# Kernel optimization log

Measured on AMD Instinct MI355X. Metric: run time of the kernel, lower is better.

The kernel has to match this reference:

```python
import jax, jax.numpy as jnp
import numpy as np

# Model constants (match init_kwargs)
H = 16       # num query heads
HKV = 8      # num kv heads
G = H // HKV # group size for GQA
D = 128      # head_dim
EPS = 1e-06
THETA = 10000.0
SCALE = D ** -0.5


def setup_inputs() -> dict:
    key = jax.random.key(0)
    k1, k2, k3 = jax.random.split(key, 3)
    T, HID = 2048, 2048
    qkv_out = H * D + 2 * HKV * D  # 4096
    return {
        "x": jax.random.normal(k1, (T, HID), jnp.float32),
        "pos": jnp.arange(T, dtype=jnp.int64 if jax.config.jax_enable_x64 else jnp.int32),
        "w_qkv": jax.random.normal(k2, (HID, qkv_out), jnp.float32) * 0.02,
        "q_norm_w": jnp.ones((D,), jnp.float32),
        "k_norm_w": jnp.ones((D,), jnp.float32),
        "w_o": jax.random.normal(k3, (H * D, HID), jnp.float32) * 0.02,
    }


def _rmsnorm(x, w):
    # per-head RMSNorm over last dim (head_dim)
    var = jnp.mean(jnp.square(x), axis=-1, keepdims=True)
    return x * jax.lax.rsqrt(var + EPS) * w


def _rope(x, pos):
    # neox-style rotary: rotate_half over full head_dim
    inv_freq = 1.0 / (THETA ** (jnp.arange(0, D, 2, dtype=jnp.float32) / D))  # [D/2]
    ang = pos.astype(jnp.float32)[:, None] * inv_freq                          # [T, D/2]
    cos = jnp.concatenate([jnp.cos(ang), jnp.cos(ang)], -1)[:, None, :]        # [T,1,D]
    sin = jnp.concatenate([jnp.sin(ang), jnp.sin(ang)], -1)[:, None, :]
    x1, x2 = x[..., : D // 2], x[..., D // 2 :]
    rot = jnp.concatenate([-x2, x1], -1)
    return x * cos + rot * sin


def reference(x, pos, w_qkv, q_norm_w, k_norm_w, w_o):
    T = x.shape[0]
    qkv = x @ w_qkv                                   # [T, (H+2*HKV)*D]
    q = qkv[:, : H * D].reshape(T, H, D)
    k = qkv[:, H * D : (H + HKV) * D].reshape(T, HKV, D)
    v = qkv[:, (H + HKV) * D :].reshape(T, HKV, D)
    q = _rmsnorm(q, q_norm_w)
    k = _rmsnorm(k, k_norm_w)
    q = _rope(q, pos)
    k = _rope(k, pos)
    # GQA causal attention over a single flattened sequence
    qg = q.reshape(T, HKV, G, D)
    scores = jnp.einsum("qhgd,khd->hgqk", qg, k) * SCALE   # [HKV,G,T,T]
    causal = pos[:, None] >= pos[None, :]                   # [T,T]
    scores = jnp.where(causal, scores, jnp.finfo(scores.dtype).min)
    probs = jax.nn.softmax(scores, axis=-1)
    o = jnp.einsum("hgqk,khd->qhgd", probs, v).reshape(T, H * D)
    return o @ w_o
```

## Files before the change

kernel.cpp:

```cpp
#include <hip/hip_runtime.h>
#include <hip/hip_bf16.h>
#include <math.h>

#define T_SEQ 2048
#define HID   2048
#define NH    16
#define NKV   8
#define DH    128
#define QKV_N 4096
#define KOFF  2048
#define VOFF  3072
#define EPS_RMS 1e-6f
#define ATT_SCALE 0.08838834764831845f

typedef __attribute__((ext_vector_type(8))) short bf16x8;
typedef __attribute__((ext_vector_type(4))) float f32x4;
typedef unsigned short u16;

__device__ __forceinline__ u16 f2b(float f) {
  union { float f; unsigned u; } v; v.f = f;
  unsigned r = v.u + 0x7fff + ((v.u >> 16) & 1);
  return (u16)(r >> 16);
}
__device__ __forceinline__ float b2f(u16 x) {
  union { unsigned u; float f; } v; v.u = ((unsigned)x) << 16;
  return v.f;
}

__device__ __forceinline__ void g2l16(u16* l, const u16* g) {
#if __has_builtin(__builtin_amdgcn_global_load_lds)
  __builtin_amdgcn_global_load_lds(
      (const __attribute__((address_space(1))) unsigned int*)g,
      (__attribute__((address_space(3))) unsigned int*)l, 16, 0, 0);
#else
  *(float4*)l = *(const float4*)g;
#endif
}

__global__ __launch_bounds__(256)
void cast_bf16(const float* __restrict__ src, u16* __restrict__ dst) {
  const int i = blockIdx.x * 256 + threadIdx.x;
  const float4 v = ((const float4*)src)[i];
  ushort4 o; o.x = f2b(v.x); o.y = f2b(v.y); o.z = f2b(v.z); o.w = f2b(v.w);
  ((ushort4*)dst)[i] = o;
}

__global__ __launch_bounds__(256)
void tcast(const float* __restrict__ src, u16* __restrict__ dst, int R, int C) {
  __shared__ u16 tile[32][36];
  const int br = blockIdx.y * 32, bc = blockIdx.x * 32;
  const int t = threadIdx.x;
  {
    const int r = t >> 3, c4 = (t & 7) * 4;
    const float4 v = *(const float4*)(src + (size_t)(br + r) * C + bc + c4);
    tile[c4 + 0][r] = f2b(v.x);
    tile[c4 + 1][r] = f2b(v.y);
    tile[c4 + 2][r] = f2b(v.z);
    tile[c4 + 3][r] = f2b(v.w);
  }
  __syncthreads();
  {
    const int c = t >> 3, r4 = (t & 7) * 4;
    ushort4 o = { tile[c][r4], tile[c][r4 + 1], tile[c][r4 + 2], tile[c][r4 + 3] };
    *(ushort4*)(dst + (size_t)(bc + c) * R + br + r4) = o;
  }
}

template<int BOUT>
__global__ __launch_bounds__(256)
void gemm_bt(const u16* __restrict__ A, const u16* __restrict__ BT,
             void* __restrict__ Cout, int M, int N, int K) {
  __shared__ u16 sA[128 * 32];
  __shared__ u16 sB[128 * 32];

  const int t = threadIdx.x;
  const int lane = t & 63, wv = t >> 6;
  const int lo = lane & 15, hi = lane >> 4;
  const int bm = blockIdx.y * 128, bn = blockIdx.x * 128;
  const int wr = (wv >> 1) * 64, wc = (wv & 1) * 64;

  f32x4 acc[4][4];
#pragma unroll
  for (int m = 0; m < 4; ++m)
#pragma unroll
    for (int n = 0; n < 4; ++n) acc[m][n] = (f32x4){0.f, 0.f, 0.f, 0.f};

  const int arow = wv * 32 + (lane >> 2);
  const int koff = (lane & 3) * 8;
  const u16* gA = A + (size_t)(bm + arow) * K + koff;
  const u16* gB = BT + (size_t)(bn + arow) * K + koff;
  u16* lA = sA + wv * 1024 + lane * 8;
  u16* lB = sB + wv * 1024 + lane * 8;

  for (int k0 = 0; k0 < K; k0 += 32) {
    g2l16(lA,       gA + k0);
    g2l16(lA + 512, gA + (size_t)16 * K + k0);
    g2l16(lB,       gB + k0);
    g2l16(lB + 512, gB + (size_t)16 * K + k0);
    __syncthreads();

    bf16x8 af[4], bfr[4];
#pragma unroll
    for (int m = 0; m < 4; ++m)
      af[m] = *(const bf16x8*)(sA + (wr + m * 16 + lo) * 32 + hi * 8);
#pragma unroll
    for (int n = 0; n < 4; ++n)
      bfr[n] = *(const bf16x8*)(sB + (wc + n * 16 + lo) * 32 + hi * 8);
#pragma unroll
    for (int m = 0; m < 4; ++m)
#pragma unroll
      for (int n = 0; n < 4; ++n)
        acc[m][n] = __builtin_amdgcn_mfma_f32_16x16x32_bf16(af[m], bfr[n], acc[m][n], 0, 0, 0);
    __syncthreads();
  }

#pragma unroll
  for (int m = 0; m < 4; ++m)
#pragma unroll
    for (int n = 0; n < 4; ++n)
#pragma unroll
      for (int r = 0; r < 4; ++r) {
        const int row = bm + wr + m * 16 + hi * 4 + r;
        const int col = bn + wc + n * 16 + lo;
        if constexpr (BOUT)
          ((u16*)Cout)[(size_t)row * N + col] = f2b(acc[m][n][r]);
        else
          ((float*)Cout)[(size_t)row * N + col] = acc[m][n][r];
      }
}

__global__ __launch_bounds__(256)
void normrope(const u16* __restrict__ qkvb, const int* __restrict__ pos,
              const float* __restrict__ qw, const float* __restrict__ kw,
              u16* __restrict__ qbf, u16* __restrict__ kbf) {
  const int wv = threadIdx.x >> 6, lane = threadIdx.x & 63;
  const int idx = blockIdx.x * 4 + wv;
  const int tt = idx / 24, hh = idx % 24;

  const int off = (hh < NH) ? hh * DH : KOFF + (hh - NH) * DH;
  const u16* base = qkvb + (size_t)tt * QKV_N + off;
  const float x1 = b2f(base[lane]);
  const float x2 = b2f(base[lane + 64]);

  float ss = x1 * x1 + x2 * x2;
#pragma unroll
  for (int o = 32; o > 0; o >>= 1) ss += __shfl_xor(ss, o);

  const float inv = rsqrtf(ss * (1.0f / DH) + EPS_RMS);
  const float* w = (hh < NH) ? qw : kw;
  const float n1 = x1 * inv * w[lane];
  const float n2 = x2 * inv * w[lane + 64];

  const float p    = (float)pos[tt];
  const float freq = exp2f((float)lane * -0.20762050593046014f);
  const float ang  = p * freq;
  const float c = cosf(ang), s = sinf(ang);
  const float o1 = n1 * c - n2 * s;
  const float o2 = n2 * c + n1 * s;

  if (hh < NH) {
    u16* dst = qbf + ((size_t)tt * NH + hh) * DH;
    dst[lane]      = f2b(o1);
    dst[lane + 64] = f2b(o2);
  } else {
    const int u = (tt & 7) << 3;
    u16* dst = kbf + ((size_t)tt * NKV + (hh - NH)) * DH;
    dst[lane ^ u]        = f2b(o1);
    dst[(lane ^ u) + 64] = f2b(o2);
  }
}

__global__ __launch_bounds__(256)
void vtrans(const u16* __restrict__ qkvb, u16* __restrict__ vT) {
  __shared__ u16 td[128][40];
  const int kvh = blockIdx.y;
  const int t0  = blockIdx.x * 32;
  const int f   = threadIdx.x;
  {
    const int r = f >> 3, c0 = (f & 7) * 16;
    const u16* src = qkvb + (size_t)(t0 + r) * QKV_N + VOFF + kvh * DH + c0;
    bf16x8 a = *(const bf16x8*)src;
    bf16x8 b = *(const bf16x8*)(src + 8);
#pragma unroll
    for (int j = 0; j < 8; ++j) td[c0 + j][r]     = ((u16*)&a)[j];
#pragma unroll
    for (int j = 0; j < 8; ++j) td[c0 + 8 + j][r] = ((u16*)&b)[j];
  }
  __syncthreads();
  {
    const int d = f >> 1, half = f & 1;
    const int sw = (d & 7) << 3;
    u16* orow = vT + (size_t)(kvh * DH + d) * T_SEQ;
#pragma unroll
    for (int g = 0; g < 2; ++g) {
      const int tb = t0 + half * 16 + g * 8;
      *(bf16x8*)(orow + (tb ^ sw)) = *(const bf16x8*)(&td[d][half * 16 + g * 8]);
    }
  }
}

__global__ __launch_bounds__(256)
void flash_mfma(const u16* __restrict__ qbf, const u16* __restrict__ kbf,
                const u16* __restrict__ vT, u16* __restrict__ obuf) {
  __shared__ u16 kls[64 * 128];
  __shared__ u16 vls[128 * 64];
  __shared__ u16 pls[4][16][72];

  const int t = threadIdx.x, lane = t & 63, wv = t >> 6;
  const int lo = lane & 15, hi = lane >> 4;

  const int id  = blockIdx.x;
  const int xcd = id & 7;
  const int idx = id >> 3;
  const int h   = xcd * 2 + (idx & 1);
  const int qt  = 31 - (idx >> 1);
  const int kvh = h >> 1;
  const int q0  = qt * 64;

  bf16x8 qf[4];
#pragma unroll
  for (int kk = 0; kk < 4; ++kk)
    qf[kk] = *(const bf16x8*)(qbf + ((size_t)(q0 + wv * 16 + lo) * NH + h) * DH
                              + kk * 32 + hi * 8);

  f32x4 oacc[8];
#pragma unroll
  for (int n = 0; n < 8; ++n) oacc[n] = (f32x4){0.f, 0.f, 0.f, 0.f};
  float mrow[4] = {-INFINITY, -INFINITY, -INFINITY, -INFINITY};
  float lrow[4] = {0.f, 0.f, 0.f, 0.f};

  auto stage_k = [&](int k0) {
#pragma unroll
    for (int c = 0; c < 4; ++c) {
      const int chunk = wv * 4 + c;
      g2l16(kls + chunk * 512 + lane * 8,
            kbf + ((size_t)(k0 + chunk * 4 + hi) * NKV + kvh) * DH + lo * 8);
    }
  };
  auto stage_v = [&](int k0) {
#pragma unroll
    for (int c = 0; c < 4; ++c) {
      const int chunk = wv * 4 + c;
      const int d = chunk * 8 + (lane >> 3);
      g2l16(vls + chunk * 512 + lane * 8,
            vT + (size_t)(kvh * DH + d) * T_SEQ + k0 + (lane & 7) * 8);
    }
  };

  stage_k(0);
  stage_v(0);
  __syncthreads();

  for (int kt = 0; kt <= qt; ++kt) {
    const int k0 = kt * 64;

    f32x4 sacc[4];
#pragma unroll
    for (int n = 0; n < 4; ++n) sacc[n] = (f32x4){0.f, 0.f, 0.f, 0.f};
    __builtin_amdgcn_s_setprio(1);
#pragma unroll
    for (int n = 0; n < 4; ++n) {
      const int r = n * 16 + lo;
      const u16* kb = kls + r * 128;
#pragma unroll
      for (int kk = 0; kk < 4; ++kk) {
        const int offs = (kk * 32 + hi * 8) ^ ((r & 7) << 3);
        bf16x8 b = *(const bf16x8*)(kb + offs);
        sacc[n] = __builtin_amdgcn_mfma_f32_16x16x32_bf16(qf[kk], b, sacc[n], 0, 0, 0);
      }
    }
    __builtin_amdgcn_s_setprio(0);

    __syncthreads();
    if (kt < qt) stage_k(k0 + 64);

    float pv[4][4], tm[4];
    const bool diag = (kt == qt);
#pragma unroll
    for (int r = 0; r < 4; ++r) {
      const int qi = q0 + wv * 16 + hi * 4 + r;
      float mx = -INFINITY;
#pragma unroll
      for (int n = 0; n < 4; ++n) {
        float s = sacc[n][r] * ATT_SCALE;
        if (diag && qi < k0 + n * 16 + lo) s = -INFINITY;
        pv[n][r] = s;
        mx = fmaxf(mx, s);
      }
      tm[r] = mx;
    }
#pragma unroll
    for (int o = 8; o > 0; o >>= 1)
#pragma unroll
      for (int r = 0; r < 4; ++r) tm[r] = fmaxf(tm[r], __shfl_xor(tm[r], o));

    float al[4], rs[4];
#pragma unroll
    for (int r = 0; r < 4; ++r) {
      const float mn = fmaxf(mrow[r], tm[r]);
      al[r] = __expf(mrow[r] - mn);
      mrow[r] = mn;
      rs[r] = 0.f;
    }
#pragma unroll
    for (int n = 0; n < 4; ++n)
#pragma unroll
      for (int r = 0; r < 4; ++r) {
        const float p = __expf(pv[n][r] - mrow[r]);
        pv[n][r] = p;
        rs[r] += p;
      }
#pragma unroll
    for (int o = 8; o > 0; o >>= 1)
#pragma unroll
      for (int r = 0; r < 4; ++r) rs[r] += __shfl_xor(rs[r], o);
#pragma unroll
    for (int r = 0; r < 4; ++r) lrow[r] = lrow[r] * al[r] + rs[r];
#pragma unroll
    for (int n = 0; n < 8; ++n)
#pragma unroll
      for (int r = 0; r < 4; ++r) oacc[n][r] *= al[r];

#pragma unroll
    for (int n = 0; n < 4; ++n)
#pragma unroll
      for (int r = 0; r < 4; ++r)
        pls[wv][hi * 4 + r][n * 16 + lo] = f2b(pv[n][r]);

    bf16x8 pa[2];
#pragma unroll
    for (int kk = 0; kk < 2; ++kk)
      pa[kk] = *(const bf16x8*)(&pls[wv][lo][kk * 32 + hi * 8]);
    __builtin_amdgcn_s_setprio(1);
#pragma unroll
    for (int n = 0; n < 8; ++n) {
      const int d = n * 16 + lo;
      const u16* vb = vls + d * 64;
#pragma unroll
      for (int kk = 0; kk < 2; ++kk) {
        const int offs = (kk * 32 + hi * 8) ^ ((d & 7) << 3);
        bf16x8 b = *(const bf16x8*)(vb + offs);
        oacc[n] = __builtin_amdgcn_mfma_f32_16x16x32_bf16(pa[kk], b, oacc[n], 0, 0, 0);
      }
    }
    __builtin_amdgcn_s_setprio(0);

    __syncthreads();
    if (kt < qt) stage_v(k0 + 64);
  }

  float inv[4];
#pragma unroll
  for (int r = 0; r < 4; ++r) inv[r] = 1.0f / lrow[r];
#pragma unroll
  for (int n = 0; n < 8; ++n)
#pragma unroll
    for (int r = 0; r < 4; ++r)
      obuf[(size_t)(q0 + wv * 16 + hi * 4 + r) * HID + h * DH + n * 16 + lo] =
          f2b(oacc[n][r] * inv[r]);
}

extern "C" void kernel_launch(void* const* d_in, const int* in_sizes, int n_in,
                              void* d_out, int out_size, void* d_ws, size_t ws_size,
                              hipStream_t stream) {
  const float* x     = (const float*)d_in[0];
  const int*   pos   = (const int*)d_in[1];
  const float* w_qkv = (const float*)d_in[2];
  const float* qw    = (const float*)d_in[3];
  const float* kw    = (const float*)d_in[4];
  const float* w_o   = (const float*)d_in[5];
  float* out = (float*)d_out;

  char* w = (char*)d_ws;
  u16* xbf   = (u16*)w;
  u16* qbf   = xbf;
  u16* wqkvT = (u16*)(w + 8388608);
  u16* kbf   = wqkvT;
  u16* vTb   = wqkvT + 2097152;
  u16* obuf  = wqkvT + 4194304;
  u16* woT   = (u16*)(w + 25165824);
  u16* qkvbf = (u16*)(w + 33554432);

  cast_bf16<<<T_SEQ * HID / 4 / 256, 256, 0, stream>>>(x, xbf);
  tcast<<<dim3(QKV_N / 32, HID / 32), 256, 0, stream>>>(w_qkv, wqkvT, HID, QKV_N);
  tcast<<<dim3(HID / 32, HID / 32), 256, 0, stream>>>(w_o, woT, HID, HID);

  gemm_bt<1><<<dim3(QKV_N / 128, T_SEQ / 128), 256, 0, stream>>>(
      xbf, wqkvT, qkvbf, T_SEQ, QKV_N, HID);

  normrope<<<T_SEQ * 24 / 4, 256, 0, stream>>>(qkvbf, pos, qw, kw, qbf, kbf);
  vtrans<<<dim3(T_SEQ / 32, NKV), 256, 0, stream>>>(qkvbf, vTb);

  flash_mfma<<<dim3(T_SEQ / 64 * NH), 256, 0, stream>>>(qbf, kbf, vTb, obuf);

  gemm_bt<0><<<dim3(HID / 128, T_SEQ / 128), 256, 0, stream>>>(
      obuf, woT, out, T_SEQ, HID, HID);
}
```

Measured before the change: 302.2 us.

## Split long causal query tiles across two blocks and merge partial softmax results

The 24 longest query tiles per head (qt 8..31) are now split over the KV range into two halves, each processed by its own block. Partial outputs go to a workspace buffer in bf16 together with the row max and sum, and a new merge kernel combines them with log-sum-exp rescaling. Short tiles still run in one block. The aim is to cut the load imbalance and tail of the causal attention grid, at the cost of an extra launch, extra global traffic and bf16 rounding of the unnormalized partials.

```diff
diff --git a/kernel.cpp b/kernel.cpp
--- a/kernel.cpp
+++ b/kernel.cpp
@@ -201,7 +201,8 @@
 
 __global__ __launch_bounds__(256)
 void flash_mfma(const u16* __restrict__ qbf, const u16* __restrict__ kbf,
-                const u16* __restrict__ vT, u16* __restrict__ obuf) {
+                const u16* __restrict__ vT, u16* __restrict__ obuf,
+                u16* __restrict__ pO, float* __restrict__ ml) {
   __shared__ u16 kls[64 * 128];
   __shared__ u16 vls[128 * 64];
   __shared__ u16 pls[4][16][72];
@@ -211,9 +212,18 @@
 
   const int id  = blockIdx.x;
   const int xcd = id & 7;
-  const int idx = id >> 3;
-  const int h   = xcd * 2 + (idx & 1);
-  const int qt  = 31 - (idx >> 1);
+  const int j   = id >> 3;
+  const int h   = xcd * 2 + (j & 1);
+  const int s   = j >> 1;
+  int qt, part, kt0, kt1, split;
+  if (s < 48) {
+    qt = 31 - (s >> 1); part = s & 1; split = 1;
+    const int half = (qt + 1) >> 1;
+    kt0 = part ? half : 0;
+    kt1 = part ? qt : half - 1;
+  } else {
+    qt = 55 - s; part = 0; split = 0; kt0 = 0; kt1 = qt;
+  }
   const int kvh = h >> 1;
   const int q0  = qt * 64;
 
@@ -247,11 +257,11 @@
     }
   };
 
-  stage_k(0);
-  stage_v(0);
+  stage_k(kt0 * 64);
+  stage_v(kt0 * 64);
   __syncthreads();
 
-  for (int kt = 0; kt <= qt; ++kt) {
+  for (int kt = kt0; kt <= kt1; ++kt) {
     const int k0 = kt * 64;
 
     f32x4 sacc[4];
@@ -272,7 +282,7 @@
     __builtin_amdgcn_s_setprio(0);
 
     __syncthreads();
-    if (kt < qt) stage_k(k0 + 64);
+    if (kt < kt1) stage_k(k0 + 64);
 
     float pv[4][4], tm[4];
     const bool diag = (kt == qt);
@@ -282,10 +292,10 @@
       float mx = -INFINITY;
 #pragma unroll
       for (int n = 0; n < 4; ++n) {
-        float s = sacc[n][r] * ATT_SCALE;
-        if (diag && qi < k0 + n * 16 + lo) s = -INFINITY;
-        pv[n][r] = s;
-        mx = fmaxf(mx, s);
+        float sv = sacc[n][r] * ATT_SCALE;
+        if (diag && qi < k0 + n * 16 + lo) sv = -INFINITY;
+        pv[n][r] = sv;
+        mx = fmaxf(mx, sv);
       }
       tm[r] = mx;
     }
@@ -346,18 +356,60 @@
     __builtin_amdgcn_s_setprio(0);
 
     __syncthreads();
-    if (kt < qt) stage_v(k0 + 64);
-  }
-
-  float inv[4];
-#pragma unroll
-  for (int r = 0; r < 4; ++r) inv[r] = 1.0f / lrow[r];
-#pragma unroll
-  for (int n = 0; n < 8; ++n)
-#pragma unroll
-    for (int r = 0; r < 4; ++r)
-      obuf[(size_t)(q0 + wv * 16 + hi * 4 + r) * HID + h * DH + n * 16 + lo] =
-          f2b(oacc[n][r] * inv[r]);
+    if (kt < kt1) stage_v(k0 + 64);
+  }
+
+  if (split) {
+    const size_t rbase = (size_t)(part * 16 + h) * 1536
+                       + (size_t)(qt - 8) * 64 + wv * 16;
+#pragma unroll
+    for (int n = 0; n < 8; ++n)
+#pragma unroll
+      for (int r = 0; r < 4; ++r)
+        pO[(rbase + hi * 4 + r) * 128 + n * 16 + lo] = f2b(oacc[n][r]);
+    if (lo == 0) {
+#pragma unroll
+      for (int r = 0; r < 4; ++r) {
+        ml[(rbase + hi * 4 + r) * 2 + 0] = mrow[r];
+        ml[(rbase + hi * 4 + r) * 2 + 1] = lrow[r];
+      }
+    }
+  } else {
+    float inv[4];
+#pragma unroll
+    for (int r = 0; r < 4; ++r) inv[r] = 1.0f / lrow[r];
+#pragma unroll
+    for (int n = 0; n < 8; ++n)
+#pragma unroll
+      for (int r = 0; r < 4; ++r)
+        obuf[(size_t)(q0 + wv * 16 + hi * 4 + r) * HID + h * DH + n * 16 + lo] =
+            f2b(oacc[n][r] * inv[r]);
+  }
+}
+
+__global__ __launch_bounds__(256)
+void merge_split(const u16* __restrict__ pO, const float* __restrict__ ml,
+                 u16* __restrict__ obuf) {
+  const int tid = threadIdx.x;
+  const int rl = tid >> 4, lane16 = tid & 15;
+  const int r = blockIdx.x * 16 + rl;
+  const int h = r / 1536, prow = r % 1536;
+  const int trow = 512 + prow;
+  const size_t iA = (size_t)h * 1536 + prow;
+  const size_t iB = (size_t)(16 + h) * 1536 + prow;
+  const float mA = ml[iA * 2], lA = ml[iA * 2 + 1];
+  const float mB = ml[iB * 2], lB = ml[iB * 2 + 1];
+  const float m  = fmaxf(mA, mB);
+  const float a  = __expf(mA - m), b = __expf(mB - m);
+  const float inv = 1.0f / (lA * a + lB * b);
+  const float ca = a * inv, cb = b * inv;
+  bf16x8 va = *(const bf16x8*)(pO + iA * 128 + lane16 * 8);
+  bf16x8 vb = *(const bf16x8*)(pO + iB * 128 + lane16 * 8);
+  u16 o[8];
+#pragma unroll
+  for (int k = 0; k < 8; ++k)
+    o[k] = f2b(ca * b2f(((const u16*)&va)[k]) + cb * b2f(((const u16*)&vb)[k]));
+  *(bf16x8*)(obuf + (size_t)trow * HID + h * DH + lane16 * 8) = *(bf16x8*)o;
 }
 
 extern "C" void kernel_launch(void* const* d_in, const int* in_sizes, int n_in,
@@ -380,6 +432,8 @@
   u16* obuf  = wqkvT + 4194304;
   u16* woT   = (u16*)(w + 25165824);
   u16* qkvbf = (u16*)(w + 33554432);
+  u16*   pO  = (u16*)(w + 33554432);
+  float* ml  = (float*)(w + 46137344);
 
   cast_bf16<<<T_SEQ * HID / 4 / 256, 256, 0, stream>>>(x, xbf);
   tcast<<<dim3(QKV_N / 32, HID / 32), 256, 0, stream>>>(w_qkv, wqkvT, HID, QKV_N);
@@ -391,7 +445,8 @@
   normrope<<<T_SEQ * 24 / 4, 256, 0, stream>>>(qkvbf, pos, qw, kw, qbf, kbf);
   vtrans<<<dim3(T_SEQ / 32, NKV), 256, 0, stream>>>(qkvbf, vTb);
 
-  flash_mfma<<<dim3(T_SEQ / 64 * NH), 256, 0, stream>>>(qbf, kbf, vTb, obuf);
+  flash_mfma<<<896, 256, 0, stream>>>(qbf, kbf, vTb, obuf, pO, ml);
+  merge_split<<<1536, 256, 0, stream>>>(pO, ml, obuf);
 
   gemm_bt<0><<<dim3(HID / 128, T_SEQ / 128), 256, 0, stream>>>(
       obuf, woT, out, T_SEQ, HID, HID);
```

Result: faster. 285.5 us (-5.5%).
